# Performance work log

Hardware: AMD Instinct MI355X
Metric: run time of the kernel (lower is better)

## Reference

```python
import jax, jax.numpy as jnp
import numpy as np

K = 4            # branching factor of the complete dependency tree
LEVELS = 8       # depths 0..7
N = (K**LEVELS - 1) // (K - 1)   # 21845 nodes, levels stored contiguously
D = 128
NUM_POS = 18     # universal POS tags -> pos_params ModuleList size
NUM_DEP = 46     # dependency relations -> dep_params ModuleList size


def level_start(l):
    # index of first node at depth l (breadth-first layout)
    return (K**l - 1) // (K - 1)


def setup_inputs() -> dict:
    key = jax.random.key(0)
    ks = jax.random.split(key, 7)
    emb = jax.random.normal(ks[0], (N, D), jnp.float32)
    pos_ids = jax.random.randint(ks[1], (N,), 0, NUM_POS)
    dep_ids = jax.random.randint(ks[2], (N,), 0, NUM_DEP)  # dep tag of edge to parent
    s = 1.0 / np.sqrt(D)  # torch nn.Linear default init range
    pos_W = jax.random.uniform(ks[3], (NUM_POS, D, D), jnp.float32, -s, s)
    pos_b = jax.random.uniform(ks[4], (NUM_POS, D), jnp.float32, -s, s)
    dep_W = jax.random.uniform(ks[5], (NUM_DEP, D, D), jnp.float32, -s, s)
    dep_b = jax.random.uniform(ks[6], (NUM_DEP, D), jnp.float32, -s, s)
    return {"emb": emb, "pos_ids": pos_ids, "dep_ids": dep_ids,
            "pos_W": pos_W, "pos_b": pos_b, "dep_W": dep_W, "dep_b": dep_b}


def reference(emb, pos_ids, dep_ids, pos_W, pos_b, dep_W, dep_b) -> jnp.ndarray:
    # x_i = relu(PosLinear_{pos_i}(emb_i)) for every node (batched typed linear
    # via per-node weight gather: the memory-bound gather this module implies)
    x = jax.nn.relu(jnp.einsum('nd,nde->ne', emb, pos_W[pos_ids]) + pos_b[pos_ids])

    # bottom-up level sweep; leaves have no children so z = x there
    lo = level_start(LEVELS - 1)
    z = x[lo:lo + K**(LEVELS - 1)]            # [n_leaf, D]
    for l in range(LEVELS - 2, -1, -1):
        cs = level_start(l + 1)
        n_c = K**(l + 1)
        did = dep_ids[cs:cs + n_c]
        # z_c -> relu(DepLinear_{dep_c}(z_c)) for every child of this level
        u = jax.nn.relu(jnp.einsum('nd,nde->ne', z, dep_W[did]) + dep_b[did])
        # max over the K children of each parent, then max with parent's x
        u = u.reshape(K**l, K, D).max(axis=1)
        s = level_start(l)
        z = jnp.maximum(x[s:s + K**l], u)
    return z[0]  # root sentence embedding [D]
```

## Files before the change

kernel.cpp:

```cpp
#include <hip/hip_runtime.h>


#define DD 128
#define NN 21845
#define NPOS 18
#define NDEP 46
#define NCH 21844
#define NBUCKET 340

typedef __attribute__((ext_vector_type(8))) short short8;
typedef __attribute__((ext_vector_type(4))) float f32x4;

__device__ __forceinline__ unsigned short f2bf(float f) {
    union { float f; unsigned int u; } v; v.f = f;
    unsigned int r = v.u + 0x7fffu + ((v.u >> 16) & 1u);
    return (unsigned short)(r >> 16);
}
__device__ __forceinline__ float bf2f(unsigned short s) {
    union { unsigned int u; float f; } v; v.u = ((unsigned int)s) << 16;
    return v.f;
}

__device__ __forceinline__ void decode_child(int j, const int* __restrict__ dep_ids,
                                             int& l, int& c, int& b) {
    int base = 0, sz = 4;
    l = 0;
    while (j >= base + sz) { base += sz; sz <<= 2; ++l; }
    c = j - base;
    int did = dep_ids[base + 1 + c];
    b = NPOS + l * NDEP + did;
}

__global__ __launch_bounds__(256) void prep_kernel(
        const float* __restrict__ posW, const float* __restrict__ depW,
        unsigned short* __restrict__ Wt,
        const int* __restrict__ pos_ids, const int* __restrict__ dep_ids,
        int* __restrict__ cnt) {
    __shared__ char smem[64 * 72 * 2];
    if (blockIdx.x < 256) {
        unsigned short (*lds)[72] = (unsigned short (*)[72])smem;
        int mat = blockIdx.x >> 2;
        int tile = blockIdx.x & 3;
        int tk = (tile >> 1) * 64, tn = (tile & 1) * 64;
        const float* W = (mat < NPOS) ? (posW + (size_t)mat * DD * DD)
                                      : (depW + (size_t)(mat - NPOS) * DD * DD);
        unsigned short* O = Wt + (size_t)mat * DD * DD;
        int tx = threadIdx.x & 63, ty = threadIdx.x >> 6;
#pragma unroll
        for (int i = 0; i < 16; ++i) {
            int r = ty + i * 4;
            lds[tx][r] = f2bf(W[(size_t)(tk + r) * DD + tn + tx]);
        }
        __syncthreads();
#pragma unroll
        for (int i = 0; i < 16; ++i) {
            int r = ty + i * 4;
            O[(size_t)(tn + r) * DD + tk + tx] = lds[r][tx];
        }
    } else {
        int* h = (int*)smem;
        for (int i = threadIdx.x; i < NBUCKET; i += 256) h[i] = 0;
        __syncthreads();
        int g = (blockIdx.x - 256) * 256 + threadIdx.x;
        if (g < NN) {
            atomicAdd(&h[pos_ids[g]], 1);
        } else if (g < NN + NCH) {
            int l, c, b;
            decode_child(g - NN, dep_ids, l, c, b);
            atomicAdd(&h[b], 1);
        }
        __syncthreads();
        for (int i = threadIdx.x; i < NBUCKET; i += 256) {
            int v = h[i];
            if (v) atomicAdd(&cnt[i], v);
        }
    }
}

__global__ void scan_kernel(const int* __restrict__ cnt, int* __restrict__ cur,
                            int* __restrict__ ntiles, int2* __restrict__ tbl1,
                            int2* __restrict__ tblL) {
    int w = threadIdx.x >> 6;
    int lane = threadIdx.x & 63;
    if (lane != 0) return;
    if (w == 0) {
        int off = 0, t = 0;
        for (int b = 0; b < NPOS; ++b) {
            int c = cnt[b];
            cur[b] = off;
            for (int rs = 0; rs < c; rs += 64) {
                int rr = min(64, c - rs);
                tbl1[t].x = b | (rr << 8);
                tbl1[t].y = off + rs;
                ++t;
            }
            off += c;
        }
        ntiles[0] = t;
    } else {
        int l = w - 1;
        const int baseTab[7] = {0, 4, 20, 84, 340, 1364, 5460};
        int base = baseTab[l];
        int off = 0, t = 0;
        int2* tb = tblL + l * 302;
        for (int b = 0; b < NDEP; ++b) {
            int c = cnt[NPOS + l * NDEP + b];
            cur[NPOS + l * NDEP + b] = base + off;
            for (int rs = 0; rs < c; rs += 64) {
                int rr = min(64, c - rs);
                tb[t].x = b | (rr << 8);
                tb[t].y = base + off + rs;
                ++t;
            }
            off += c;
        }
        ntiles[1 + l] = t;
    }
}

__global__ __launch_bounds__(256) void scatter_kernel(
        const int* __restrict__ pos_ids, const int* __restrict__ dep_ids,
        int* __restrict__ cur, int* __restrict__ perm_pos,
        int* __restrict__ perm_dep) {
    __shared__ int h[NBUCKET];
    __shared__ int base[NBUCKET];
    for (int i = threadIdx.x; i < NBUCKET; i += 256) h[i] = 0;
    __syncthreads();
    int g = blockIdx.x * 256 + threadIdx.x;
    int b = -1, payload = 0;
    if (g < NN) {
        b = pos_ids[g];
        payload = g;
    } else if (g < NN + NCH) {
        int l, c;
        decode_child(g - NN, dep_ids, l, c, b);
        payload = c;
    }
    int local = 0;
    if (b >= 0) local = atomicAdd(&h[b], 1);
    __syncthreads();
    for (int i = threadIdx.x; i < NBUCKET; i += 256) {
        int v = h[i];
        if (v) base[i] = atomicAdd(&cur[i], v);
    }
    __syncthreads();
    if (b >= 0) {
        int idx = base[b] + local;
        if (b < NPOS) perm_pos[idx] = payload;
        else perm_dep[idx] = payload;
    }
}

template <int MODE>
__global__ __launch_bounds__(256) void gemm_kernel(
        const int2* __restrict__ tbl, const int* __restrict__ ntp,
        const int* __restrict__ perm, const unsigned short* __restrict__ Wt,
        const float* __restrict__ bias, const float* __restrict__ embf,
        const unsigned short* __restrict__ xb, const unsigned short* __restrict__ uprev,
        unsigned short* __restrict__ outr) {
    int nt = ntp[0];
    if ((int)blockIdx.x >= nt) return;
    int2 e = tbl[blockIdx.x];
    int bucket = e.x & 255;
    int rows = e.x >> 8;
    int rowstart = e.y;
    int lane = threadIdx.x & 63;
    int w = threadIdx.x >> 6;
    int lr = lane & 15;
    int kk = (lane >> 4) * 8;

    const short8 zero8 = {0, 0, 0, 0, 0, 0, 0, 0};

    int m_a = w * 16 + lr;
    bool valid_a = m_a < rows;
    int rid_a = valid_a ? perm[rowstart + m_a] : 0;

    short8 afr[4];
    if (MODE == 0) {
        const float* ar = embf + (size_t)rid_a * DD + kk;
#pragma unroll
        for (int s = 0; s < 4; ++s) {
            float4 lo = *(const float4*)(ar + s * 32);
            float4 hi = *(const float4*)(ar + s * 32 + 4);
            short8 a;
            a[0] = (short)f2bf(lo.x); a[1] = (short)f2bf(lo.y);
            a[2] = (short)f2bf(lo.z); a[3] = (short)f2bf(lo.w);
            a[4] = (short)f2bf(hi.x); a[5] = (short)f2bf(hi.y);
            a[6] = (short)f2bf(hi.z); a[7] = (short)f2bf(hi.w);
            afr[s] = valid_a ? a : zero8;
        }
    } else if (MODE == 1) {
        const unsigned short* ar = xb + (size_t)rid_a * DD + kk;
#pragma unroll
        for (int s = 0; s < 4; ++s)
            afr[s] = valid_a ? *(const short8*)(ar + s * 32) : zero8;
    } else {
        const unsigned short* xr = xb + (size_t)rid_a * DD + kk;
        const unsigned short* ur = uprev + (size_t)(4 * rid_a) * DD + kk;
#pragma unroll
        for (int s = 0; s < 4; ++s) {
            short8 a = *(const short8*)(xr + s * 32);
#pragma unroll
            for (int j = 0; j < 4; ++j) {
                short8 u = *(const short8*)(ur + j * DD + s * 32);
#pragma unroll
                for (int q = 0; q < 8; ++q)
                    if ((unsigned short)u[q] > (unsigned short)a[q]) a[q] = u[q];
            }
            afr[s] = valid_a ? a : zero8;
        }
    }

    f32x4 acc[8];
#pragma unroll
    for (int t = 0; t < 8; ++t) acc[t] = (f32x4){0.f, 0.f, 0.f, 0.f};

    const unsigned short* Wb = Wt + (size_t)bucket * DD * DD;
#pragma unroll
    for (int s = 0; s < 4; ++s) {
        short8 bfr[8];
#pragma unroll
        for (int t = 0; t < 8; ++t)
            bfr[t] = *(const short8*)(Wb + (size_t)(t * 16 + lr) * DD + s * 32 + kk);
#pragma unroll
        for (int t = 0; t < 8; ++t)
            acc[t] = __builtin_amdgcn_mfma_f32_16x16x32_bf16(afr[s], bfr[t], acc[t], 0, 0, 0);
    }

    int rq[4]; bool vq[4];
#pragma unroll
    for (int q = 0; q < 4; ++q) {
        int m = w * 16 + (lane >> 4) * 4 + q;
        vq[q] = m < rows;
        rq[q] = vq[q] ? perm[rowstart + m] : 0;
    }
    const float* bb = bias + bucket * DD;
#pragma unroll
    for (int t = 0; t < 8; ++t) {
        int col = t * 16 + lr;
        float bv = bb[col];
#pragma unroll
        for (int q = 0; q < 4; ++q) {
            if (vq[q]) {
                float v = fmaxf(acc[t][q] + bv, 0.f);
                outr[(size_t)rq[q] * DD + col] = f2bf(v);
            }
        }
    }
}

__global__ void final_kernel(const unsigned short* __restrict__ xb,
                             const unsigned short* __restrict__ u0,
                             float* __restrict__ out) {
    int e = threadIdx.x;
    unsigned short m = xb[e];
#pragma unroll
    for (int j = 0; j < 4; ++j) {
        unsigned short u = u0[j * DD + e];
        if (u > m) m = u;
    }
    out[e] = bf2f(m);
}

extern "C" void kernel_launch(void* const* d_in, const int* in_sizes, int n_in,
                              void* d_out, int out_size, void* d_ws, size_t ws_size,
                              hipStream_t stream) {
    const float* emb     = (const float*)d_in[0];
    const int*   pos_ids = (const int*)d_in[1];
    const int*   dep_ids = (const int*)d_in[2];
    const float* pos_W   = (const float*)d_in[3];
    const float* pos_b   = (const float*)d_in[4];
    const float* dep_W   = (const float*)d_in[5];
    const float* dep_b   = (const float*)d_in[6];
    float* out = (float*)d_out;

    char* p = (char*)d_ws;
    auto alloc = [&](size_t bytes) {
        char* r = p; p += (bytes + 255) & ~(size_t)255; return r;
    };
    unsigned short* xbf = (unsigned short*)alloc((size_t)NN * DD * 2);
    unsigned short* uA  = (unsigned short*)alloc((size_t)16384 * DD * 2);
    unsigned short* uB  = (unsigned short*)alloc((size_t)4096 * DD * 2);
    unsigned short* Wt  = (unsigned short*)alloc((size_t)64 * DD * DD * 2);
    int*  cnt      = (int*)alloc(NBUCKET * 4);
    int*  cur      = (int*)alloc(NBUCKET * 4);
    int*  ntiles   = (int*)alloc(8 * 4);
    int*  perm_pos = (int*)alloc((size_t)NN * 4);
    int*  perm_dep = (int*)alloc((size_t)NCH * 4);
    int2* tbl1     = (int2*)alloc(360 * 8);
    int2* tblL     = (int2*)alloc(7 * 302 * 8);

    hipMemsetAsync(cnt, 0, NBUCKET * 4, stream);
    prep_kernel<<<256 + 171, 256, 0, stream>>>(pos_W, dep_W, Wt, pos_ids, dep_ids, cnt);
    scan_kernel<<<1, 512, 0, stream>>>(cnt, cur, ntiles, tbl1, tblL);
    scatter_kernel<<<171, 256, 0, stream>>>(pos_ids, dep_ids, cur, perm_pos, perm_dep);

    gemm_kernel<0><<<360, 256, 0, stream>>>(tbl1, ntiles + 0, perm_pos, Wt, pos_b,
                                            emb, nullptr, nullptr, xbf);

    const unsigned short* Wtd = Wt + (size_t)NPOS * DD * DD;
    gemm_kernel<1><<<302, 256, 0, stream>>>(tblL + 6 * 302, ntiles + 7, perm_dep, Wtd,
                                            dep_b, nullptr, xbf + (size_t)5461 * DD,
                                            nullptr, uA);
    const int ls_c[7]  = {1, 5, 21, 85, 341, 1365, 5461};
    const int grids[7] = {4, 16, 47, 50, 62, 110, 302};
    unsigned short* uin = uA;
    unsigned short* uout = uB;
    for (int l = 5; l >= 0; --l) {
        gemm_kernel<2><<<grids[l], 256, 0, stream>>>(tblL + l * 302, ntiles + 1 + l,
                                                     perm_dep, Wtd, dep_b, nullptr,
                                                     xbf + (size_t)ls_c[l] * DD, uin, uout);
        unsigned short* t = uin; uin = uout; uout = t;
    }
    final_kernel<<<1, 128, 0, stream>>>(xbf, uin, out);
}
```

Before: 201.2 us.

## Fuse all pipeline stages into one persistent kernel with grid barriers

Replaces the eleven separate launches (prep, scan, scatter, pos GEMM, seven level GEMMs, final) with a single persistent kernel of 432 blocks. Stages are separated by a two-level atomic grid barrier, which removes per-launch gaps between the many small, latency-bound level kernels. The serial scan is also rewritten as a wave-parallel shuffle prefix sum. The design relies on all 432 blocks being co-resident for the barrier to avoid deadlock, and it adds twelve barrier round trips.

```diff
diff --git a/kernel.cpp b/kernel.cpp
--- a/kernel.cpp
+++ b/kernel.cpp
@@ -7,6 +7,8 @@
 #define NDEP 46
 #define NCH 21844
 #define NBUCKET 340
+#define GRID 432
+#define NBAR 12
 
 typedef __attribute__((ext_vector_type(8))) short short8;
 typedef __attribute__((ext_vector_type(4))) float f32x4;
@@ -31,136 +33,31 @@
     b = NPOS + l * NDEP + did;
 }
 
-__global__ __launch_bounds__(256) void prep_kernel(
-        const float* __restrict__ posW, const float* __restrict__ depW,
-        unsigned short* __restrict__ Wt,
-        const int* __restrict__ pos_ids, const int* __restrict__ dep_ids,
-        int* __restrict__ cnt) {
-    __shared__ char smem[64 * 72 * 2];
-    if (blockIdx.x < 256) {
-        unsigned short (*lds)[72] = (unsigned short (*)[72])smem;
-        int mat = blockIdx.x >> 2;
-        int tile = blockIdx.x & 3;
-        int tk = (tile >> 1) * 64, tn = (tile & 1) * 64;
-        const float* W = (mat < NPOS) ? (posW + (size_t)mat * DD * DD)
-                                      : (depW + (size_t)(mat - NPOS) * DD * DD);
-        unsigned short* O = Wt + (size_t)mat * DD * DD;
-        int tx = threadIdx.x & 63, ty = threadIdx.x >> 6;
-#pragma unroll
-        for (int i = 0; i < 16; ++i) {
-            int r = ty + i * 4;
-            lds[tx][r] = f2bf(W[(size_t)(tk + r) * DD + tn + tx]);
-        }
-        __syncthreads();
-#pragma unroll
-        for (int i = 0; i < 16; ++i) {
-            int r = ty + i * 4;
-            O[(size_t)(tn + r) * DD + tk + tx] = lds[r][tx];
-        }
-    } else {
-        int* h = (int*)smem;
-        for (int i = threadIdx.x; i < NBUCKET; i += 256) h[i] = 0;
-        __syncthreads();
-        int g = (blockIdx.x - 256) * 256 + threadIdx.x;
-        if (g < NN) {
-            atomicAdd(&h[pos_ids[g]], 1);
-        } else if (g < NN + NCH) {
-            int l, c, b;
-            decode_child(g - NN, dep_ids, l, c, b);
-            atomicAdd(&h[b], 1);
-        }
-        __syncthreads();
-        for (int i = threadIdx.x; i < NBUCKET; i += 256) {
-            int v = h[i];
-            if (v) atomicAdd(&cnt[i], v);
-        }
-    }
-}
-
-__global__ void scan_kernel(const int* __restrict__ cnt, int* __restrict__ cur,
-                            int* __restrict__ ntiles, int2* __restrict__ tbl1,
-                            int2* __restrict__ tblL) {
-    int w = threadIdx.x >> 6;
-    int lane = threadIdx.x & 63;
-    if (lane != 0) return;
-    if (w == 0) {
-        int off = 0, t = 0;
-        for (int b = 0; b < NPOS; ++b) {
-            int c = cnt[b];
-            cur[b] = off;
-            for (int rs = 0; rs < c; rs += 64) {
-                int rr = min(64, c - rs);
-                tbl1[t].x = b | (rr << 8);
-                tbl1[t].y = off + rs;
-                ++t;
+__device__ __forceinline__ void gridbar(int* c0, int* c1, int* gen, int idx) {
+    __syncthreads();
+    if (threadIdx.x == 0) {
+        __threadfence();
+        int g = blockIdx.x >> 4;
+        if (atomicAdd(&c0[(idx * 27 + g) * 16], 1) == 15) {
+            if (atomicAdd(&c1[idx * 16], 1) == 26) {
+                __hip_atomic_store(gen, idx + 1, __ATOMIC_RELEASE,
+                                   __HIP_MEMORY_SCOPE_AGENT);
             }
-            off += c;
-        }
-        ntiles[0] = t;
-    } else {
-        int l = w - 1;
-        const int baseTab[7] = {0, 4, 20, 84, 340, 1364, 5460};
-        int base = baseTab[l];
-        int off = 0, t = 0;
-        int2* tb = tblL + l * 302;
-        for (int b = 0; b < NDEP; ++b) {
-            int c = cnt[NPOS + l * NDEP + b];
-            cur[NPOS + l * NDEP + b] = base + off;
-            for (int rs = 0; rs < c; rs += 64) {
-                int rr = min(64, c - rs);
-                tb[t].x = b | (rr << 8);
-                tb[t].y = base + off + rs;
-                ++t;
-            }
-            off += c;
-        }
-        ntiles[1 + l] = t;
-    }
-}
-
-__global__ __launch_bounds__(256) void scatter_kernel(
-        const int* __restrict__ pos_ids, const int* __restrict__ dep_ids,
-        int* __restrict__ cur, int* __restrict__ perm_pos,
-        int* __restrict__ perm_dep) {
-    __shared__ int h[NBUCKET];
-    __shared__ int base[NBUCKET];
-    for (int i = threadIdx.x; i < NBUCKET; i += 256) h[i] = 0;
+        }
+        while (__hip_atomic_load(gen, __ATOMIC_RELAXED,
+                                 __HIP_MEMORY_SCOPE_AGENT) < idx + 1)
+            __builtin_amdgcn_s_sleep(4);
+        __threadfence();
+    }
     __syncthreads();
-    int g = blockIdx.x * 256 + threadIdx.x;
-    int b = -1, payload = 0;
-    if (g < NN) {
-        b = pos_ids[g];
-        payload = g;
-    } else if (g < NN + NCH) {
-        int l, c;
-        decode_child(g - NN, dep_ids, l, c, b);
-        payload = c;
-    }
-    int local = 0;
-    if (b >= 0) local = atomicAdd(&h[b], 1);
-    __syncthreads();
-    for (int i = threadIdx.x; i < NBUCKET; i += 256) {
-        int v = h[i];
-        if (v) base[i] = atomicAdd(&cur[i], v);
-    }
-    __syncthreads();
-    if (b >= 0) {
-        int idx = base[b] + local;
-        if (b < NPOS) perm_pos[idx] = payload;
-        else perm_dep[idx] = payload;
-    }
 }
 
 template <int MODE>
-__global__ __launch_bounds__(256) void gemm_kernel(
-        const int2* __restrict__ tbl, const int* __restrict__ ntp,
-        const int* __restrict__ perm, const unsigned short* __restrict__ Wt,
+__device__ __forceinline__ void gemm_tile(
+        int2 e, const int* __restrict__ perm, const unsigned short* __restrict__ Wt,
         const float* __restrict__ bias, const float* __restrict__ embf,
         const unsigned short* __restrict__ xb, const unsigned short* __restrict__ uprev,
         unsigned short* __restrict__ outr) {
-    int nt = ntp[0];
-    if ((int)blockIdx.x >= nt) return;
-    int2 e = tbl[blockIdx.x];
     int bucket = e.x & 255;
     int rows = e.x >> 8;
     int rowstart = e.y;
@@ -168,7 +65,6 @@
     int w = threadIdx.x >> 6;
     int lr = lane & 15;
     int kk = (lane >> 4) * 8;
-
     const short8 zero8 = {0, 0, 0, 0, 0, 0, 0, 0};
 
     int m_a = w * 16 + lr;
@@ -249,17 +145,152 @@
     }
 }
 
-__global__ void final_kernel(const unsigned short* __restrict__ xb,
-                             const unsigned short* __restrict__ u0,
-                             float* __restrict__ out) {
-    int e = threadIdx.x;
-    unsigned short m = xb[e];
-#pragma unroll
-    for (int j = 0; j < 4; ++j) {
-        unsigned short u = u0[j * DD + e];
-        if (u > m) m = u;
-    }
-    out[e] = bf2f(m);
+__global__ __launch_bounds__(256, 2) void mega_kernel(
+        const float* __restrict__ emb, const int* __restrict__ pos_ids,
+        const int* __restrict__ dep_ids, const float* __restrict__ posW,
+        const float* __restrict__ pos_b, const float* __restrict__ depW,
+        const float* __restrict__ dep_b, float* __restrict__ out,
+        int* __restrict__ cnt, int* __restrict__ c0, int* __restrict__ c1,
+        int* __restrict__ gen, int* __restrict__ cur, int* __restrict__ ntiles,
+        int* __restrict__ perm_pos, int* __restrict__ perm_dep,
+        int2* __restrict__ tbl1, int2* __restrict__ tblL,
+        unsigned short* __restrict__ Wt, unsigned short* __restrict__ xbf,
+        unsigned short* __restrict__ uA, unsigned short* __restrict__ uB) {
+    __shared__ char smem[9232];
+    int bid = blockIdx.x;
+    int tid = threadIdx.x;
+
+    if (bid < 256) {
+        unsigned short (*lds)[72] = (unsigned short (*)[72])smem;
+        int mat = bid >> 2;
+        int tile = bid & 3;
+        int tk = (tile >> 1) * 64, tn = (tile & 1) * 64;
+        const float* W = (mat < NPOS) ? (posW + (size_t)mat * DD * DD)
+                                      : (depW + (size_t)(mat - NPOS) * DD * DD);
+        unsigned short* O = Wt + (size_t)mat * DD * DD;
+        int tx = tid & 63, ty = tid >> 6;
+#pragma unroll
+        for (int i = 0; i < 16; ++i) {
+            int r = ty + i * 4;
+            lds[tx][r] = f2bf(W[(size_t)(tk + r) * DD + tn + tx]);
+        }
+        __syncthreads();
+#pragma unroll
+        for (int i = 0; i < 16; ++i) {
+            int r = ty + i * 4;
+            O[(size_t)(tn + r) * DD + tk + tx] = lds[r][tx];
+        }
+    } else if (bid < 427) {
+        int* h = (int*)smem;
+        for (int i = tid; i < NBUCKET; i += 256) h[i] = 0;
+        __syncthreads();
+        int g = (bid - 256) * 256 + tid;
+        if (g < NN) {
+            atomicAdd(&h[pos_ids[g]], 1);
+        } else if (g < NN + NCH) {
+            int l, c, b;
+            decode_child(g - NN, dep_ids, l, c, b);
+            atomicAdd(&h[b], 1);
+        }
+        __syncthreads();
+        for (int i = tid; i < NBUCKET; i += 256) {
+            int v = h[i];
+            if (v) atomicAdd(&cnt[i], v);
+        }
+    }
+    gridbar(c0, c1, gen, 0);
+
+    if (bid < 8 && tid < 64) {
+        int grp = bid;
+        int NB = (grp == 0) ? NPOS : NDEP;
+        int cntoff = (grp == 0) ? 0 : NPOS + (grp - 1) * NDEP;
+        int base = 0;
+        if (grp > 0) { int l = grp - 1; base = ((1 << (2 * l + 2)) - 4) / 3; }
+        int2* tb = (grp == 0) ? tbl1 : tblL + (grp - 1) * 302;
+        int lane = tid;
+        int c = (lane < NB) ? cnt[cntoff + lane] : 0;
+        int t = (c + 63) >> 6;
+        int pi = c, qi = t;
+#pragma unroll
+        for (int off = 1; off < 64; off <<= 1) {
+            int a = __shfl_up(pi, off);
+            int b2 = __shfl_up(qi, off);
+            if (lane >= off) { pi += a; qi += b2; }
+        }
+        int pe = pi - c, qe = qi - t;
+        if (lane < NB) {
+            cur[cntoff + lane] = base + pe;
+            for (int k = 0; k < t; ++k) {
+                int rr = min(64, c - (k << 6));
+                int2 ent; ent.x = lane | (rr << 8); ent.y = base + pe + (k << 6);
+                tb[qe + k] = ent;
+            }
+            if (lane == NB - 1) ntiles[grp] = qi;
+        }
+    }
+    gridbar(c0, c1, gen, 1);
+
+    if (bid < 171) {
+        int* h = (int*)smem;
+        int* basep = h + NBUCKET;
+        for (int i = tid; i < NBUCKET; i += 256) h[i] = 0;
+        __syncthreads();
+        int g = bid * 256 + tid;
+        int b = -1, payload = 0;
+        if (g < NN) {
+            b = pos_ids[g]; payload = g;
+        } else if (g < NN + NCH) {
+            int l, c;
+            decode_child(g - NN, dep_ids, l, c, b);
+            payload = c;
+        }
+        int local = 0;
+        if (b >= 0) local = atomicAdd(&h[b], 1);
+        __syncthreads();
+        for (int i = tid; i < NBUCKET; i += 256) {
+            int v = h[i];
+            if (v) basep[i] = atomicAdd(&cur[i], v);
+        }
+        __syncthreads();
+        if (b >= 0) {
+            int idx = basep[b] + local;
+            if (b < NPOS) perm_pos[idx] = payload;
+            else perm_dep[idx] = payload;
+        }
+    }
+    gridbar(c0, c1, gen, 2);
+
+    if (bid < ntiles[0])
+        gemm_tile<0>(tbl1[bid], perm_pos, Wt, pos_b, emb, nullptr, nullptr, xbf);
+    gridbar(c0, c1, gen, 3);
+
+    const unsigned short* Wtd = Wt + (size_t)NPOS * DD * DD;
+    if (bid < ntiles[7])
+        gemm_tile<1>(tblL[6 * 302 + bid], perm_dep, Wtd, dep_b, nullptr,
+                     xbf + (size_t)5461 * DD, nullptr, uA);
+    gridbar(c0, c1, gen, 4);
+
+    unsigned short* uin = uA;
+    unsigned short* uout = uB;
+    int baridx = 5;
+    for (int l = 5; l >= 0; --l) {
+        int lsc = ((1 << (2 * l + 2)) - 1) / 3;
+        if (bid < ntiles[1 + l])
+            gemm_tile<2>(tblL[l * 302 + bid], perm_dep, Wtd, dep_b, nullptr,
+                         xbf + (size_t)lsc * DD, uin, uout);
+        gridbar(c0, c1, gen, baridx++);
+        unsigned short* tswap = uin; uin = uout; uout = tswap;
+    }
+
+    if (bid == 0 && tid < DD) {
+        unsigned short m = xbf[tid];
+#pragma unroll
+        for (int j = 0; j < 4; ++j) {
+            unsigned short u = uin[j * DD + tid];
+            if (u > m) m = u;
+        }
+        out[tid] = bf2f(m);
+    }
 }
 
 extern "C" void kernel_launch(void* const* d_in, const int* in_sizes, int n_in,
@@ -278,39 +309,27 @@
     auto alloc = [&](size_t bytes) {
         char* r = p; p += (bytes + 255) & ~(size_t)255; return r;
     };
-    unsigned short* xbf = (unsigned short*)alloc((size_t)NN * DD * 2);
-    unsigned short* uA  = (unsigned short*)alloc((size_t)16384 * DD * 2);
-    unsigned short* uB  = (unsigned short*)alloc((size_t)4096 * DD * 2);
-    unsigned short* Wt  = (unsigned short*)alloc((size_t)64 * DD * DD * 2);
-    int*  cnt      = (int*)alloc(NBUCKET * 4);
+    int* meta = (int*)alloc((340 + NBAR * 27 * 16 + NBAR * 16 + 1) * 4);
+    int* cnt = meta;
+    int* c0  = meta + 340;
+    int* c1  = c0 + NBAR * 27 * 16;
+    int* gen = c1 + NBAR * 16;
+    size_t meta_bytes = (size_t)(340 + NBAR * 27 * 16 + NBAR * 16 + 1) * 4;
+
     int*  cur      = (int*)alloc(NBUCKET * 4);
     int*  ntiles   = (int*)alloc(8 * 4);
     int*  perm_pos = (int*)alloc((size_t)NN * 4);
     int*  perm_dep = (int*)alloc((size_t)NCH * 4);
     int2* tbl1     = (int2*)alloc(360 * 8);
     int2* tblL     = (int2*)alloc(7 * 302 * 8);
-
-    hipMemsetAsync(cnt, 0, NBUCKET * 4, stream);
-    prep_kernel<<<256 + 171, 256, 0, stream>>>(pos_W, dep_W, Wt, pos_ids, dep_ids, cnt);
-    scan_kernel<<<1, 512, 0, stream>>>(cnt, cur, ntiles, tbl1, tblL);
-    scatter_kernel<<<171, 256, 0, stream>>>(pos_ids, dep_ids, cur, perm_pos, perm_dep);
-
-    gemm_kernel<0><<<360, 256, 0, stream>>>(tbl1, ntiles + 0, perm_pos, Wt, pos_b,
-                                            emb, nullptr, nullptr, xbf);
-
-    const unsigned short* Wtd = Wt + (size_t)NPOS * DD * DD;
-    gemm_kernel<1><<<302, 256, 0, stream>>>(tblL + 6 * 302, ntiles + 7, perm_dep, Wtd,
-                                            dep_b, nullptr, xbf + (size_t)5461 * DD,
-                                            nullptr, uA);
-    const int ls_c[7]  = {1, 5, 21, 85, 341, 1365, 5461};
-    const int grids[7] = {4, 16, 47, 50, 62, 110, 302};
-    unsigned short* uin = uA;
-    unsigned short* uout = uB;
-    for (int l = 5; l >= 0; --l) {
-        gemm_kernel<2><<<grids[l], 256, 0, stream>>>(tblL + l * 302, ntiles + 1 + l,
-                                                     perm_dep, Wtd, dep_b, nullptr,
-                                                     xbf + (size_t)ls_c[l] * DD, uin, uout);
-        unsigned short* t = uin; uin = uout; uout = t;
-    }
-    final_kernel<<<1, 128, 0, stream>>>(xbf, uin, out);
-}
+    unsigned short* Wt  = (unsigned short*)alloc((size_t)64 * DD * DD * 2);
+    unsigned short* xbf = (unsigned short*)alloc((size_t)NN * DD * 2);
+    unsigned short* uA  = (unsigned short*)alloc((size_t)16384 * DD * 2);
+    unsigned short* uB  = (unsigned short*)alloc((size_t)4096 * DD * 2);
+
+    hipMemsetAsync(meta, 0, meta_bytes, stream);
+    mega_kernel<<<GRID, 256, 0, stream>>>(emb, pos_ids, dep_ids, pos_W, pos_b,
+                                          dep_W, dep_b, out, cnt, c0, c1, gen,
+                                          cur, ntiles, perm_pos, perm_dep,
+                                          tbl1, tblL, Wt, xbf, uA, uB);
+}
```

Measured after the change: 334.0 us. +66.0%, slower.

## Merge bucketing prep into one kernel and fold top tree levels into tail kernel

Applied to the files above, without the earlier changes.

The histogram, scan and scatter steps are folded into block 0 of the prep kernel, which does all of the bucketing in shared memory. This removes the memset and two launches. The two smallest tree levels (16 and 4 children) now run in a single-block fp32 tail kernel, which reads the dep weights directly and also produces the final root max, replacing two tiny GEMM launches and the final kernel. In exchange, a single 1024-thread block handles all ~43k items serially, which may lengthen the critical path while the weight-transpose blocks run alongside it.

```diff
diff --git a/kernel.cpp b/kernel.cpp
--- a/kernel.cpp
+++ b/kernel.cpp
@@ -5,8 +5,10 @@
 #define NN 21845
 #define NPOS 18
 #define NDEP 46
-#define NCH 21844
-#define NBUCKET 340
+#define NB 248
+#define NCHALL 21844
+#define CH_LO 20
+#define NITEMS (NN + NCHALL - CH_LO)
 
 typedef __attribute__((ext_vector_type(8))) short short8;
 typedef __attribute__((ext_vector_type(4))) float f32x4;
@@ -21,131 +23,100 @@
     return v.f;
 }
 
-__device__ __forceinline__ void decode_child(int j, const int* __restrict__ dep_ids,
-                                             int& l, int& c, int& b) {
-    int base = 0, sz = 4;
-    l = 0;
-    while (j >= base + sz) { base += sz; sz <<= 2; ++l; }
-    c = j - base;
-    int did = dep_ids[base + 1 + c];
-    b = NPOS + l * NDEP + did;
-}
-
-__global__ __launch_bounds__(256) void prep_kernel(
+__global__ __launch_bounds__(1024) void prep_kernel(
         const float* __restrict__ posW, const float* __restrict__ depW,
         unsigned short* __restrict__ Wt,
         const int* __restrict__ pos_ids, const int* __restrict__ dep_ids,
-        int* __restrict__ cnt) {
-    __shared__ char smem[64 * 72 * 2];
-    if (blockIdx.x < 256) {
+        int* __restrict__ perm_pos, int* __restrict__ perm_dep,
+        int* __restrict__ ntiles, int2* __restrict__ tbl1,
+        int2* __restrict__ tblL) {
+    __shared__ __align__(16) char smem[9216];
+    int bid = blockIdx.x, tid = threadIdx.x;
+    if (bid >= 1) {
         unsigned short (*lds)[72] = (unsigned short (*)[72])smem;
-        int mat = blockIdx.x >> 2;
-        int tile = blockIdx.x & 3;
+        int mb = bid - 1;
+        int mat = mb >> 2, tile = mb & 3;
         int tk = (tile >> 1) * 64, tn = (tile & 1) * 64;
         const float* W = (mat < NPOS) ? (posW + (size_t)mat * DD * DD)
                                       : (depW + (size_t)(mat - NPOS) * DD * DD);
         unsigned short* O = Wt + (size_t)mat * DD * DD;
-        int tx = threadIdx.x & 63, ty = threadIdx.x >> 6;
-#pragma unroll
-        for (int i = 0; i < 16; ++i) {
-            int r = ty + i * 4;
+        int tx = tid & 63, ty = tid >> 6;
+#pragma unroll
+        for (int i = 0; i < 4; ++i) {
+            int r = i * 16 + ty;
             lds[tx][r] = f2bf(W[(size_t)(tk + r) * DD + tn + tx]);
         }
         __syncthreads();
 #pragma unroll
-        for (int i = 0; i < 16; ++i) {
-            int r = ty + i * 4;
+        for (int i = 0; i < 4; ++i) {
+            int r = i * 16 + ty;
             O[(size_t)(tn + r) * DD + tk + tx] = lds[r][tx];
         }
-    } else {
-        int* h = (int*)smem;
-        for (int i = threadIdx.x; i < NBUCKET; i += 256) h[i] = 0;
-        __syncthreads();
-        int g = (blockIdx.x - 256) * 256 + threadIdx.x;
+        return;
+    }
+    int* cnt  = (int*)smem;
+    int* scb  = cnt + NB;
+    int* tpre = scb + NB;
+    int* rank = tpre + NB;
+    for (int i = tid; i < NB; i += 1024) { cnt[i] = 0; rank[i] = 0; }
+    __syncthreads();
+    for (int g = tid; g < NITEMS; g += 1024) {
+        int b;
         if (g < NN) {
-            atomicAdd(&h[pos_ids[g]], 1);
-        } else if (g < NN + NCH) {
-            int l, c, b;
-            decode_child(g - NN, dep_ids, l, c, b);
-            atomicAdd(&h[b], 1);
-        }
-        __syncthreads();
-        for (int i = threadIdx.x; i < NBUCKET; i += 256) {
-            int v = h[i];
-            if (v) atomicAdd(&cnt[i], v);
-        }
-    }
-}
-
-__global__ void scan_kernel(const int* __restrict__ cnt, int* __restrict__ cur,
-                            int* __restrict__ ntiles, int2* __restrict__ tbl1,
-                            int2* __restrict__ tblL) {
-    int w = threadIdx.x >> 6;
-    int lane = threadIdx.x & 63;
-    if (lane != 0) return;
-    if (w == 0) {
-        int off = 0, t = 0;
-        for (int b = 0; b < NPOS; ++b) {
-            int c = cnt[b];
-            cur[b] = off;
-            for (int rs = 0; rs < c; rs += 64) {
-                int rr = min(64, c - rs);
-                tbl1[t].x = b | (rr << 8);
-                tbl1[t].y = off + rs;
-                ++t;
-            }
-            off += c;
-        }
-        ntiles[0] = t;
-    } else {
-        int l = w - 1;
-        const int baseTab[7] = {0, 4, 20, 84, 340, 1364, 5460};
-        int base = baseTab[l];
-        int off = 0, t = 0;
-        int2* tb = tblL + l * 302;
-        for (int b = 0; b < NDEP; ++b) {
-            int c = cnt[NPOS + l * NDEP + b];
-            cur[NPOS + l * NDEP + b] = base + off;
-            for (int rs = 0; rs < c; rs += 64) {
-                int rr = min(64, c - rs);
-                tb[t].x = b | (rr << 8);
-                tb[t].y = base + off + rs;
-                ++t;
-            }
-            off += c;
-        }
-        ntiles[1 + l] = t;
-    }
-}
-
-__global__ __launch_bounds__(256) void scatter_kernel(
-        const int* __restrict__ pos_ids, const int* __restrict__ dep_ids,
-        int* __restrict__ cur, int* __restrict__ perm_pos,
-        int* __restrict__ perm_dep) {
-    __shared__ int h[NBUCKET];
-    __shared__ int base[NBUCKET];
-    for (int i = threadIdx.x; i < NBUCKET; i += 256) h[i] = 0;
+            b = pos_ids[g];
+        } else {
+            int j = g - NN + CH_LO;
+            int base = CH_LO, sz = 64, l = 2;
+            while (j >= base + sz) { base += sz; sz <<= 2; ++l; }
+            int c = j - base;
+            b = NPOS + (l - 2) * NDEP + dep_ids[base + 1 + c];
+        }
+        atomicAdd(&cnt[b], 1);
+    }
     __syncthreads();
-    int g = blockIdx.x * 256 + threadIdx.x;
-    int b = -1, payload = 0;
-    if (g < NN) {
-        b = pos_ids[g];
-        payload = g;
-    } else if (g < NN + NCH) {
-        int l, c;
-        decode_child(g - NN, dep_ids, l, c, b);
-        payload = c;
-    }
-    int local = 0;
-    if (b >= 0) local = atomicAdd(&h[b], 1);
+    if (tid == 0) {
+        const int gb[6] = {0, 20, 84, 340, 1364, 5460};
+        int b = 0;
+        for (int g = 0; g < 6; ++g) {
+            int w = (g == 0) ? NPOS : NDEP;
+            int off = gb[g], tp = 0;
+            for (int i = 0; i < w; ++i, ++b) {
+                scb[b] = off; tpre[b] = tp;
+                off += cnt[b]; tp += (cnt[b] + 63) >> 6;
+            }
+            ntiles[g] = tp;
+        }
+    }
     __syncthreads();
-    for (int i = threadIdx.x; i < NBUCKET; i += 256) {
-        int v = h[i];
-        if (v) base[i] = atomicAdd(&cur[i], v);
+    if (tid < NB) {
+        int b = tid;
+        int g = (b < NPOS) ? 0 : 1 + (b - NPOS) / NDEP;
+        int loc = (b < NPOS) ? b : (b - NPOS) % NDEP;
+        int2* tb = (g == 0) ? tbl1 : tblL + (g - 1) * 302;
+        int c = cnt[b];
+        int t = (c + 63) >> 6;
+        for (int k = 0; k < t; ++k) {
+            int2 ent;
+            ent.x = loc | (min(64, c - (k << 6)) << 8);
+            ent.y = scb[b] + (k << 6);
+            tb[tpre[b] + k] = ent;
+        }
     }
     __syncthreads();
-    if (b >= 0) {
-        int idx = base[b] + local;
+    for (int g = tid; g < NITEMS; g += 1024) {
+        int b, payload;
+        if (g < NN) {
+            b = pos_ids[g]; payload = g;
+        } else {
+            int j = g - NN + CH_LO;
+            int base = CH_LO, sz = 64, l = 2;
+            while (j >= base + sz) { base += sz; sz <<= 2; ++l; }
+            int c = j - base;
+            b = NPOS + (l - 2) * NDEP + dep_ids[base + 1 + c];
+            payload = c;
+        }
+        int r = atomicAdd(&rank[b], 1);
+        int idx = scb[b] + r;
         if (b < NPOS) perm_pos[idx] = payload;
         else perm_dep[idx] = payload;
     }
@@ -168,7 +139,6 @@
     int w = threadIdx.x >> 6;
     int lr = lane & 15;
     int kk = (lane >> 4) * 8;
-
     const short8 zero8 = {0, 0, 0, 0, 0, 0, 0, 0};
 
     int m_a = w * 16 + lr;
@@ -249,17 +219,69 @@
     }
 }
 
-__global__ void final_kernel(const unsigned short* __restrict__ xb,
-                             const unsigned short* __restrict__ u0,
-                             float* __restrict__ out) {
-    int e = threadIdx.x;
-    unsigned short m = xb[e];
-#pragma unroll
-    for (int j = 0; j < 4; ++j) {
-        unsigned short u = u0[j * DD + e];
-        if (u > m) m = u;
-    }
-    out[e] = bf2f(m);
+__global__ __launch_bounds__(1024) void tail_kernel(
+        const int* __restrict__ dep_ids, const float* __restrict__ depW,
+        const float* __restrict__ dep_b, const unsigned short* __restrict__ xbf,
+        unsigned short* __restrict__ uarena, float* __restrict__ out) {
+    __shared__ float zbuf[8][DD];
+    int team = threadIdx.x >> 7, e = threadIdx.x & 127;
+    {
+        const unsigned short* up = uarena + (size_t)21760 * DD;
+        unsigned short* uc = uarena + (size_t)21824 * DD;
+        for (int rnd = 0; rnd < 2; ++rnd) {
+            int c = team + rnd * 8;
+            unsigned short m = xbf[(size_t)(5 + c) * DD + e];
+#pragma unroll
+            for (int j = 0; j < 4; ++j) {
+                unsigned short u = up[(size_t)(4 * c + j) * DD + e];
+                if (u > m) m = u;
+            }
+            zbuf[team][e] = bf2f(m);
+            __syncthreads();
+            int did = dep_ids[5 + c];
+            const float* W = depW + (size_t)did * DD * DD;
+            float a = dep_b[did * DD + e];
+#pragma unroll 8
+            for (int k = 0; k < DD; ++k)
+                a = fmaf(zbuf[team][k], W[(size_t)k * DD + e], a);
+            uc[(size_t)c * DD + e] = f2bf(fmaxf(a, 0.f));
+            __syncthreads();
+        }
+    }
+    {
+        const unsigned short* up = uarena + (size_t)21824 * DD;
+        unsigned short* uc = uarena + (size_t)21840 * DD;
+        int c = team;
+        if (team < 4) {
+            unsigned short m = xbf[(size_t)(1 + c) * DD + e];
+#pragma unroll
+            for (int j = 0; j < 4; ++j) {
+                unsigned short u = up[(size_t)(4 * c + j) * DD + e];
+                if (u > m) m = u;
+            }
+            zbuf[team][e] = bf2f(m);
+        }
+        __syncthreads();
+        if (team < 4) {
+            int did = dep_ids[1 + c];
+            const float* W = depW + (size_t)did * DD * DD;
+            float a = dep_b[did * DD + e];
+#pragma unroll 8
+            for (int k = 0; k < DD; ++k)
+                a = fmaf(zbuf[team][k], W[(size_t)k * DD + e], a);
+            uc[(size_t)c * DD + e] = f2bf(fmaxf(a, 0.f));
+        }
+        __syncthreads();
+    }
+    if (threadIdx.x < DD) {
+        unsigned short m = xbf[threadIdx.x];
+#pragma unroll
+        for (int j = 0; j < 4; ++j) {
+            unsigned short u = uarena[(size_t)(21840 + j) * DD + threadIdx.x];
+            if (u > m) m = u;
+        }
+        out[threadIdx.x] = bf2f(m);
+    }
 }
 
 extern "C" void kernel_launch(void* const* d_in, const int* in_sizes, int n_in,
@@ -278,39 +300,42 @@
     auto alloc = [&](size_t bytes) {
         char* r = p; p += (bytes + 255) & ~(size_t)255; return r;
     };
-    unsigned short* xbf = (unsigned short*)alloc((size_t)NN * DD * 2);
-    unsigned short* uA  = (unsigned short*)alloc((size_t)16384 * DD * 2);
-    unsigned short* uB  = (unsigned short*)alloc((size_t)4096 * DD * 2);
-    unsigned short* Wt  = (unsigned short*)alloc((size_t)64 * DD * DD * 2);
-    int*  cnt      = (int*)alloc(NBUCKET * 4);
-    int*  cur      = (int*)alloc(NBUCKET * 4);
     int*  ntiles   = (int*)alloc(8 * 4);
     int*  perm_pos = (int*)alloc((size_t)NN * 4);
-    int*  perm_dep = (int*)alloc((size_t)NCH * 4);
+    int*  perm_dep = (int*)alloc((size_t)NCHALL * 4);
     int2* tbl1     = (int2*)alloc(360 * 8);
-    int2* tblL     = (int2*)alloc(7 * 302 * 8);
-
-    hipMemsetAsync(cnt, 0, NBUCKET * 4, stream);
-    prep_kernel<<<256 + 171, 256, 0, stream>>>(pos_W, dep_W, Wt, pos_ids, dep_ids, cnt);
-    scan_kernel<<<1, 512, 0, stream>>>(cnt, cur, ntiles, tbl1, tblL);
-    scatter_kernel<<<171, 256, 0, stream>>>(pos_ids, dep_ids, cur, perm_pos, perm_dep);
-
+    int2* tblL     = (int2*)alloc(5 * 302 * 8);
+    unsigned short* Wt     = (unsigned short*)alloc((size_t)64 * DD * DD * 2);
+    unsigned short* xbf    = (unsigned short*)alloc((size_t)NN * DD * 2);
+    unsigned short* uarena = (unsigned short*)alloc((size_t)NCHALL * DD * 2);
+
+    prep_kernel<<<257, 1024, 0, stream>>>(pos_W, dep_W, Wt, pos_ids, dep_ids,
+                                          perm_pos, perm_dep, ntiles, tbl1, tblL);
     gemm_kernel<0><<<360, 256, 0, stream>>>(tbl1, ntiles + 0, perm_pos, Wt, pos_b,
                                             emb, nullptr, nullptr, xbf);
-
     const unsigned short* Wtd = Wt + (size_t)NPOS * DD * DD;
-    gemm_kernel<1><<<302, 256, 0, stream>>>(tblL + 6 * 302, ntiles + 7, perm_dep, Wtd,
-                                            dep_b, nullptr, xbf + (size_t)5461 * DD,
-                                            nullptr, uA);
-    const int ls_c[7]  = {1, 5, 21, 85, 341, 1365, 5461};
-    const int grids[7] = {4, 16, 47, 50, 62, 110, 302};
-    unsigned short* uin = uA;
-    unsigned short* uout = uB;
-    for (int l = 5; l >= 0; --l) {
-        gemm_kernel<2><<<grids[l], 256, 0, stream>>>(tblL + l * 302, ntiles + 1 + l,
-                                                     perm_dep, Wtd, dep_b, nullptr,
-                                                     xbf + (size_t)ls_c[l] * DD, uin, uout);
-        unsigned short* t = uin; uin = uout; uout = t;
-    }
-    final_kernel<<<1, 128, 0, stream>>>(xbf, uin, out);
-}
+    gemm_kernel<1><<<302, 256, 0, stream>>>(tblL + 4 * 302, ntiles + 5, perm_dep,
+                                            Wtd, dep_b, nullptr,
+                                            xbf + (size_t)5461 * DD, nullptr,
+                                            uarena);
+    gemm_kernel<2><<<110, 256, 0, stream>>>(tblL + 3 * 302, ntiles + 4, perm_dep,
+                                            Wtd, dep_b, nullptr,
+                                            xbf + (size_t)1365 * DD, uarena,
+                                            uarena + (size_t)16384 * DD);
+    gemm_kernel<2><<<62, 256, 0, stream>>>(tblL + 2 * 302, ntiles + 3, perm_dep,
+                                           Wtd, dep_b, nullptr,
+                                           xbf + (size_t)341 * DD,
+                                           uarena + (size_t)16384 * DD,
+                                           uarena + (size_t)20480 * DD);
+    gemm_kernel<2><<<50, 256, 0, stream>>>(tblL + 1 * 302, ntiles + 2, perm_dep,
+                                           Wtd, dep_b, nullptr,
+                                           xbf + (size_t)85 * DD,
+                                           uarena + (size_t)20480 * DD,
+                                           uarena + (size_t)21504 * DD);
+    gemm_kernel<2><<<46, 256, 0, stream>>>(tblL + 0 * 302, ntiles + 1, perm_dep,
+                                           Wtd, dep_b, nullptr,
+                                           xbf + (size_t)21 * DD,
+                                           uarena + (size_t)21504 * DD,
+                                           uarena + (size_t)21760 * DD);
+    tail_kernel<<<1, 1024, 0, stream>>>(dep_ids, dep_W, dep_b, xbf, uarena, out);
+}
```

Result: slower. 209.7 us (+4.2%).
